# Optimization experiments

Measured on AMD Instinct MI355X. Metric: run time of the kernel, lower is better.

Reference implementation:

```python
import jax, jax.numpy as jnp
import numpy as np

N_WAY = 5
K_SHOT = 5
TEMPERATURE = 1.0
NEG = -1e9  # emulates 'column does not exist' for pad columns beyond umask_length
EPS = 1e-12  # matches torch F.normalize eps


def _l2n(x, axis):
    n = jnp.sqrt(jnp.sum(x * x, axis=axis, keepdims=True))
    return x / jnp.maximum(n, EPS)


def setup_inputs() -> dict:
    key = jax.random.key(0)
    k1, k2, k3, k4, k5 = jax.random.split(key, 5)
    b, c, h, w = 4, 64, 5, 5
    q, u = 75, 100
    support_xf = jax.random.normal(k1, (b, N_WAY * K_SHOT, c, h, w), jnp.float32)
    query_xf = jax.random.normal(k2, (b, q, c, h, w), jnp.float32)
    unlabeled_xf = jax.random.normal(k3, (b, u, c, h, w), jnp.float32)
    support_y = jax.random.randint(k4, (b, N_WAY * K_SHOT), 0, N_WAY)
    query_y = jax.random.randint(k5, (b, q), 0, N_WAY)
    return {"support_xf": support_xf, "support_y": support_y, "query_xf": query_xf,
            "query_y": query_y, "unlabeled_xf": unlabeled_xf}


def _forward(support_xf, query_xf, unlabeled_xf, query_y):
    b, q, c, h, w = query_xf.shape
    M_s = K_SHOT * h * w
    unl = unlabeled_xf.reshape(b, -1, c, h, w)
    u = unl.shape[1]
    M_u = u * h * w
    # pooled unlabeled local descriptors, flattened in (u, h, w) order -> [b, c, M_u]
    unl_feat = unl.transpose(0, 2, 1, 3, 4).reshape(b, c, M_u)
    # support -> [b, n_way, c, k_shot*h*w]
    sup = support_xf.reshape(b, N_WAY, K_SHOT, c, h, w).transpose(0, 1, 3, 2, 4, 5).reshape(b, N_WAY, c, M_s)
    # cosine similarity unlabeled -> support: [b, n_way, M_u, M_s]
    u2s = jnp.einsum('bwcn,bcm->bwmn', _l2n(sup, 2), _l2n(unl_feat, 1))
    pool = u2s.transpose(0, 2, 1, 3).reshape(b, M_u, N_WAY * M_s)
    s_nearest = jnp.argmax(pool, axis=1)          # per support loc: nearest unlabeled loc
    u_nearest = jnp.argmax(pool, axis=2)          # per unlabeled loc: nearest support loc
    mutual = jnp.take_along_axis(s_nearest, u_nearest, axis=1) == jnp.arange(M_u)[None, :]  # [b, M_u]
    # class with max similarity per unlabeled location
    cls = jnp.argmax(jnp.max(u2s, axis=-1), axis=1)  # [b, M_u]
    umask = jax.nn.one_hot(cls, N_WAY, dtype=jnp.float32).transpose(0, 2, 1) \
            * mutual[:, None, :].astype(jnp.float32)  # [b, n_way, M_u]
    counts = umask.sum(-1)                          # [b, n_way]
    L = counts.max()                                # umask_length (traced)
    # stream compaction via stable argsort of the 0/1 mask (preserves original order)
    order = jnp.argsort(-umask, axis=-1)            # jnp.argsort is stable
    pts = unl_feat.transpose(0, 2, 1)               # [b, M_u, c]
    gath = jnp.take_along_axis(pts[:, None, :, :], order[..., None], axis=2)  # [b, n_way, M_u, c]
    valid = (jnp.arange(M_u)[None, None, :] < counts[:, :, None]).astype(jnp.float32)
    comp = gath * valid[..., None]                  # rows beyond count are zeros (as in torch)
    s_cat = jnp.concatenate([sup, comp.transpose(0, 1, 3, 2)], axis=-1)  # [b, n_way, c, M_s+M_u]
    M_tot = M_s + M_u
    qn = _l2n(query_xf.reshape(b, q, c, h * w), 2)
    scn = _l2n(s_cat, 2)
    sim = jnp.einsum('bqcm,bwcn->bqwmn', qn, scn)   # [b, q, n_way, M_q, M_tot]
    sim = (sim + 1.0) * 0.5                          # FourLayer_64F branch
    # columns beyond umask_length don't exist in the torch dense tensor -> exclude from maxes
    pad = jnp.arange(M_tot)[None, None, None, None, :] >= (M_s + L)
    sim = jnp.where(pad, NEG, sim)
    M_q = h * w
    qm = sim.transpose(0, 1, 3, 2, 4).reshape(b, q, M_q, N_WAY * M_tot)
    support_nearest = jnp.argmax(qm, axis=2)        # [b, q, n_way*M_tot]
    query_nearest = jnp.argmax(qm, axis=3)          # [b, q, M_q]
    g = jnp.take_along_axis(support_nearest, query_nearest, axis=2)
    q_mask = (g == jnp.arange(M_q)[None, None, :]).astype(sim.dtype)  # mutual NN mask
    query_value = (jnp.max(sim, axis=-1) * q_mask[:, :, None, :]).sum(-1)  # [b, q, n_way]
    logits = query_value.reshape(b * q, N_WAY) / TEMPERATURE
    y = query_y.reshape(b * q)
    logp = jax.nn.log_softmax(logits, axis=-1)
    loss = -jnp.take_along_axis(logp, y[:, None], axis=1).mean()
    return loss


def reference(support_xf, support_y, query_xf, query_y, unlabeled_xf):
    return _forward(support_xf, query_xf, unlabeled_xf, query_y)
```

## Files before the change

kernel.cpp:

```cpp
#include <hip/hip_runtime.h>

#define NEGINF (-1e30f)

constexpr size_t OF_UNL  = 0;
constexpr size_t OF_SUP  = OF_UNL  + (size_t)4*2500*64;
constexpr size_t OF_SUPT = OF_SUP  + (size_t)4*5*125*64;
constexpr size_t OF_QT   = OF_SUPT + (size_t)4*5*64*128;
constexpr size_t OF_ROWV = OF_QT   + (size_t)300*28*64;
constexpr size_t OF_ROWI = OF_ROWV + (size_t)4*5*8*2500;
constexpr size_t OF_CVI  = OF_ROWI + (size_t)4*5*8*2500;
constexpr size_t OF_CMP  = OF_CVI  + (size_t)4*5*125*20*2;
constexpr size_t OF_CNT  = OF_CMP  + (size_t)4*5*2500;
constexpr size_t OF_UNEAR= OF_CNT  + 20;
constexpr size_t OF_SNEAR= OF_UNEAR+ 10000;
constexpr size_t OF_BV   = OF_SNEAR+ 2500;
constexpr size_t OF_BP   = OF_BV   + 37500;
constexpr size_t OF_AMX  = OF_BP   + 37500;

typedef __attribute__((ext_vector_type(4)))  float f4s;
typedef __attribute__((ext_vector_type(16))) float f16s;

__global__ __launch_bounds__(256) void knorm(
    const float* __restrict__ sup, const float* __restrict__ qry,
    const float* __restrict__ unl,
    float* __restrict__ unl_n, float* __restrict__ sup_n,
    float* __restrict__ supT, float* __restrict__ qt)
{
    int tid = threadIdx.x;
    int lane = tid & 63, wv = tid >> 6;
    int unit = blockIdx.x * 4 + wv;

    __shared__ float ls[4][1600];
    __shared__ float scl[4][32];

    const float* src;
    float* dstT;
    float* dst2 = nullptr;
    int dst2_shot = 0;
    bool isq = false;

    if (unit < 400) {
        int b = unit / 100, u = unit % 100;
        src  = unl + (size_t)unit * 1600;
        dstT = unl_n + ((size_t)(b * 2500 + u * 25)) * 64;
    } else if (unit < 500) {
        int idx2 = unit - 400;
        int b = idx2 / 25, r = idx2 % 25;
        int w = r / 5, shot = r % 5;
        src  = sup + (size_t)(b * 25 + r) * 1600;
        dstT = sup_n + ((size_t)(b * 625 + w * 125 + shot * 25)) * 64;
        dst2 = supT + ((size_t)(b * 5 + w) * 64) * 128;
        dst2_shot = shot * 25;
    } else {
        int bq = unit - 500;
        src  = qry + (size_t)bq * 1600;
        dstT = qt + (size_t)bq * 1792;
        isq = true;
    }

    const float4* s4 = (const float4*)src;
#pragma unroll
    for (int k = 0; k < 7; ++k) {
        int idx = k * 64 + lane;
        if (idx < 400) *(float4*)&ls[wv][idx * 4] = s4[idx];
    }
    __syncthreads();

    if (lane < 25) {
        int hw = lane;
        float p[16];
#pragma unroll
        for (int sub = 0; sub < 16; ++sub) {
            float s = 0.f;
#pragma unroll
            for (int j = 0; j < 4; ++j) {
                float v = ls[wv][(sub * 4 + j) * 25 + hw];
                s += v * v;
            }
            p[sub] = s;
        }
#pragma unroll
        for (int st = 1; st < 16; st <<= 1)
#pragma unroll
            for (int i = 0; i < 16; i += 2 * st)
                p[i] = p[i] + p[i + st];
        scl[wv][hw] = 1.f / fmaxf(sqrtf(p[0]), 1e-12f);
    }
    __syncthreads();

    float4* d4 = (float4*)dstT;
#pragma unroll
    for (int k = 0; k < 7; ++k) {
        int idx = k * 64 + lane;
        if (idx < 400) {
            int f = idx * 4;
            int r_ = f >> 6;
            int c0 = f & 63;
            float m = scl[wv][r_];
            float4 o;
            o.x = ls[wv][ c0      * 25 + r_] * m;
            o.y = ls[wv][(c0 + 1) * 25 + r_] * m;
            o.z = ls[wv][(c0 + 2) * 25 + r_] * m;
            o.w = ls[wv][(c0 + 3) * 25 + r_] * m;
            d4[idx] = o;
        }
    }
    if (isq) {
        if (lane < 48) d4[400 + lane] = make_float4(0.f, 0.f, 0.f, 0.f);
    }
    if (dst2) {
#pragma unroll
        for (int k = 0; k < 25; ++k) {
            int idx = k * 64 + lane;
            int c = idx / 25, hw2 = idx % 25;
            dst2[(size_t)c * 128 + dst2_shot + hw2] = ls[wv][idx] * scl[wv][hw2];
        }
    }
}

#define KB2(C) { \
    f16s s0, s1; \
    asm volatile("s_load_dwordx16 %0, %[b], %c[o0]\n\t" \
                 "s_load_dwordx16 %1, %[b], %c[o1]\n\t" \
                 "s_waitcnt lgkmcnt(0)" \
                 : "=s"(s0), "=s"(s1) \
                 : [b]"s"(sbp), [o0]"i"((C)*512), [o1]"i"((C)*512+512)); \
    float2 uv = *(const float2*)&uls[ml * 66 + (C)]; \
    acc[0]  = fmaf(uv.x, s0[0],  fmaf(uv.y, s1[0],  acc[0])); \
    acc[1]  = fmaf(uv.x, s0[1],  fmaf(uv.y, s1[1],  acc[1])); \
    acc[2]  = fmaf(uv.x, s0[2],  fmaf(uv.y, s1[2],  acc[2])); \
    acc[3]  = fmaf(uv.x, s0[3],  fmaf(uv.y, s1[3],  acc[3])); \
    acc[4]  = fmaf(uv.x, s0[4],  fmaf(uv.y, s1[4],  acc[4])); \
    acc[5]  = fmaf(uv.x, s0[5],  fmaf(uv.y, s1[5],  acc[5])); \
    acc[6]  = fmaf(uv.x, s0[6],  fmaf(uv.y, s1[6],  acc[6])); \
    acc[7]  = fmaf(uv.x, s0[7],  fmaf(uv.y, s1[7],  acc[7])); \
    acc[8]  = fmaf(uv.x, s0[8],  fmaf(uv.y, s1[8],  acc[8])); \
    acc[9]  = fmaf(uv.x, s0[9],  fmaf(uv.y, s1[9],  acc[9])); \
    acc[10] = fmaf(uv.x, s0[10], fmaf(uv.y, s1[10], acc[10])); \
    acc[11] = fmaf(uv.x, s0[11], fmaf(uv.y, s1[11], acc[11])); \
    acc[12] = fmaf(uv.x, s0[12], fmaf(uv.y, s1[12], acc[12])); \
    acc[13] = fmaf(uv.x, s0[13], fmaf(uv.y, s1[13], acc[13])); \
    acc[14] = fmaf(uv.x, s0[14], fmaf(uv.y, s1[14], acc[14])); \
    acc[15] = fmaf(uv.x, s0[15], fmaf(uv.y, s1[15], acc[15])); }
#define KB8(C) KB2(C) KB2((C)+2) KB2((C)+4) KB2((C)+6)

__global__ __launch_bounds__(256) void kb(
    const float* __restrict__ unl_n, const float* __restrict__ supT,
    float* __restrict__ rowv, int* __restrict__ rowi, float* __restrict__ colvi)
{
    int bid = blockIdx.x;
    int nc = bid & 3;
    int mb = (bid >> 2) % 20;
    int bw = bid / 80;
    int b  = bw / 5;
    int tid = threadIdx.x;
    int lane = tid & 63, wv = tid >> 6;

    __shared__ float uls[128 * 66];
    __shared__ float sv_[4][32];
    __shared__ int   si_[4][32];

    int m0 = mb * 128;
    int n0 = nc * 32;

    for (int i = tid; i < 128 * 16; i += 256) {
        int row = i >> 4, c4 = (i & 15) * 4;
        int m = m0 + row;
        float4 x = make_float4(0.f, 0.f, 0.f, 0.f);
        if (m < 2500) x = *(const float4*)(unl_n + ((size_t)(b * 2500 + m)) * 64 + c4);
        *(float2*)&uls[row * 66 + c4]     = make_float2(x.x, x.y);
        *(float2*)&uls[row * 66 + c4 + 2] = make_float2(x.z, x.w);
    }
    __syncthreads();

    int ml = tid & 127;
    int m  = m0 + ml;
    int nh = tid >> 7;
    int nbase = nh * 16;
    int nbu = __builtin_amdgcn_readfirstlane(nbase);
    int nn_total = (125 - n0) < 32 ? (125 - n0) : 32;
    const float* sbp = supT + ((size_t)bw * 64) * 128 + n0 + nbu;

    float acc[16];
#pragma unroll
    for (int j = 0; j < 16; ++j) acc[j] = 0.f;

    KB8(0)  KB8(8)  KB8(16) KB8(24)
    KB8(32) KB8(40) KB8(48) KB8(56)

    int nnloc = nn_total - nbase;
    nnloc = nnloc < 0 ? 0 : (nnloc > 16 ? 16 : nnloc);
    float rbv = NEGINF; int rbi = 0;
    for (int j = 0; j < nnloc; ++j)
        if (acc[j] > rbv) { rbv = acc[j]; rbi = n0 + nbase + j; }
    if (m < 2500) {
        int ck = nc * 2 + nh;
        rowv[((size_t)bw * 8 + ck) * 2500 + m] = rbv;
        rowi[((size_t)bw * 8 + ck) * 2500 + m] = rbi;
    }

#pragma unroll
    for (int j = 0; j < 16; ++j) {
        float v = (m < 2500 && (nbase + j) < nn_total) ? acc[j] : NEGINF;
        float vm = v;
#pragma unroll
        for (int s2 = 1; s2 < 64; s2 <<= 1) vm = fmaxf(vm, __shfl_xor(vm, s2));
        unsigned long long msk = __ballot(v == vm);
        int first = __ffsll((unsigned long long)msk) - 1;
        if (lane == 0) { sv_[wv][nbase + j] = vm; si_[wv][nbase + j] = m0 + (wv & 1) * 64 + first; }
    }
    __syncthreads();
    if (tid < nn_total) {
        int w0 = (tid < 16) ? 0 : 2;
        float v = sv_[w0][tid];     int vi = si_[w0][tid];
        float v2 = sv_[w0 + 1][tid]; int i2 = si_[w0 + 1][tid];
        if (v2 > v || (v2 == v && i2 < vi)) { v = v2; vi = i2; }
        float* cv = colvi + ((((size_t)bw) * 125 + (n0 + tid)) * 20 + mb) * 2;
        cv[0] = v; ((int*)cv)[1] = vi;
    }
}

__global__ __launch_bounds__(64) void kmerge(
    const float* __restrict__ rowv, const int* __restrict__ rowi,
    const float* __restrict__ colvi,
    int* __restrict__ unear, int* __restrict__ snear)
{
    int it = blockIdx.x * 64 + threadIdx.x;
    if (it < 10000) {
        int b = it / 2500, m = it % 2500;
        float bv = NEGINF; int bi = 0;
#pragma unroll
        for (int w = 0; w < 5; ++w) {
#pragma unroll
            for (int ck = 0; ck < 8; ++ck) {
                size_t o = (((size_t)(b * 5 + w)) * 8 + ck) * 2500 + m;
                float v = rowv[o];
                if (v > bv) { bv = v; bi = w * 125 + rowi[o]; }
            }
        }
        unear[it] = bi;
    } else if (it < 12500) {
        int idx = it - 10000;
        const float* p = colvi + (size_t)idx * 40;
        float bv = NEGINF; int bi = 0x7fffffff;
        for (int mb2 = 0; mb2 < 20; ++mb2) {
            float v = p[mb2 * 2]; int vi = ((const int*)p)[mb2 * 2 + 1];
            if (v > bv || (v == bv && vi < bi)) { bv = v; bi = vi; }
        }
        snear[idx] = bi;
    }
}

__global__ __launch_bounds__(256) void kcmp(
    const int* __restrict__ unear, const int* __restrict__ snear,
    int* __restrict__ cmp, int* __restrict__ cntg)
{
    int p = blockIdx.x;
    int b = p / 5, way = p % 5;
    int tid = threadIdx.x, lane = tid & 63, wv = tid >> 6;
    __shared__ unsigned long long masks[40];
    __shared__ int base[40];

    for (int ch = wv; ch < 40; ch += 4) {
        int m = ch * 64 + lane;
        bool ok = false;
        if (m < 2500) {
            int un = unear[b * 2500 + m];
            ok = (un / 125 == way) && (snear[b * 625 + un] == m);
        }
        unsigned long long msk = __ballot(ok ? 1 : 0);
        if (lane == 0) masks[ch] = msk;
    }
    __syncthreads();
    if (tid == 0) {
        int s = 0;
        for (int ch = 0; ch < 40; ++ch) { base[ch] = s; s += __popcll(masks[ch]); }
        cntg[p] = s;
    }
    __syncthreads();
    for (int ch = wv; ch < 40; ch += 4) {
        unsigned long long msk = masks[ch];
        if ((msk >> lane) & 1ull) {
            int pre = __popcll(msk & ((1ull << lane) - 1ull));
            cmp[(size_t)p * 2500 + base[ch] + pre] = ch * 64 + lane;
        }
    }
}

#define QLOAD(CG, Q0,Q1,Q2,Q3,Q4,Q5,Q6) \
  asm volatile( \
    "s_load_dwordx4 %0, %[b], %c[o0]\n\t" \
    "s_load_dwordx4 %1, %[b], %c[o1]\n\t" \
    "s_load_dwordx4 %2, %[b], %c[o2]\n\t" \
    "s_load_dwordx4 %3, %[b], %c[o3]\n\t" \
    "s_load_dwordx4 %4, %[b], %c[o4]\n\t" \
    "s_load_dwordx4 %5, %[b], %c[o5]\n\t" \
    "s_load_dwordx4 %6, %[b], %c[o6]\n\t" \
    "s_waitcnt lgkmcnt(0)" \
    : "=s"(Q0), "=s"(Q1), "=s"(Q2), "=s"(Q3), "=s"(Q4), "=s"(Q5), "=s"(Q6) \
    : [b]"s"(qbp), \
      [o0]"i"((CG)*16 + 0*256), [o1]"i"((CG)*16 + 1*256), \
      [o2]"i"((CG)*16 + 2*256), [o3]"i"((CG)*16 + 3*256), \
      [o4]"i"((CG)*16 + 4*256), [o5]"i"((CG)*16 + 5*256), \
      [o6]"i"((CG)*16 + 6*256))

#define CGSTEP(CG) { \
    f4s q0,q1,q2,q3,q4,q5,q6; \
    QLOAD(CG, q0,q1,q2,q3,q4,q5,q6); \
    float4 cl = *(const float4*)&cls[lane * 68 + (CG) * 4]; \
    acc[0]=fmaf(q0.x,cl.x,fmaf(q0.y,cl.y,fmaf(q0.z,cl.z,fmaf(q0.w,cl.w,acc[0])))); \
    acc[1]=fmaf(q1.x,cl.x,fmaf(q1.y,cl.y,fmaf(q1.z,cl.z,fmaf(q1.w,cl.w,acc[1])))); \
    acc[2]=fmaf(q2.x,cl.x,fmaf(q2.y,cl.y,fmaf(q2.z,cl.z,fmaf(q2.w,cl.w,acc[2])))); \
    acc[3]=fmaf(q3.x,cl.x,fmaf(q3.y,cl.y,fmaf(q3.z,cl.z,fmaf(q3.w,cl.w,acc[3])))); \
    acc[4]=fmaf(q4.x,cl.x,fmaf(q4.y,cl.y,fmaf(q4.z,cl.z,fmaf(q4.w,cl.w,acc[4])))); \
    acc[5]=fmaf(q5.x,cl.x,fmaf(q5.y,cl.y,fmaf(q5.z,cl.z,fmaf(q5.w,cl.w,acc[5])))); \
    acc[6]=fmaf(q6.x,cl.x,fmaf(q6.y,cl.y,fmaf(q6.z,cl.z,fmaf(q6.w,cl.w,acc[6])))); }

__global__ __launch_bounds__(256) void kc1(
    const float* __restrict__ qt, const float* __restrict__ sup_n,
    const float* __restrict__ unl_n, const int* __restrict__ cmp,
    const int* __restrict__ cntg,
    float* __restrict__ bvg, int* __restrict__ bpg,
    unsigned char* __restrict__ amaxg)
{
    int bid = blockIdx.x;
    int w = bid % 5, bq = bid / 5;
    int b = bq / 75;
    int tid = threadIdx.x;
    int lane = tid & 63;
    int wvu = __builtin_amdgcn_readfirstlane(tid >> 6);
    int pbw = b * 5 + w;

    int L = 0;
#pragma unroll
    for (int i = 0; i < 20; ++i) { int v = cntg[i]; L = L > v ? L : v; }
    int cntw = 0, wb = 0;
#pragma unroll
    for (int w2 = 0; w2 < 5; ++w2) {
        int c2 = cntg[b * 5 + w2];
        if (w2 < w) wb += 125 + c2;
        if (w2 == w) cntw = c2;
    }
    int cw = 125 + cntw;

    __shared__ float cls[64 * 68];
    __shared__ float amxv[4][64];
    __shared__ int   amxg_[4][64];
    __shared__ float redv[25];
    __shared__ int   redn[25];

    const float* qbp = qt + ((size_t)bq * 28 + wvu * 7) * 64;

    float rv[7]; int rn[7];
#pragma unroll
    for (int j = 0; j < 7; ++j) { rv[j] = NEGINF; rn[j] = 0x7fffffff; }

    int nb = (cw + 63) >> 6;

    for (int b4 = 0; b4 < nb; ++b4) {
        if (b4 > 0 && tid < 64) {
            int n = (b4 - 1) * 64 + tid;
            if (n < cw) {
                float v = amxv[0][tid]; int g = amxg_[0][tid];
#pragma unroll
                for (int g2 = 1; g2 < 4; ++g2)
                    if (amxv[g2][tid] > v) { v = amxv[g2][tid]; g = amxg_[g2][tid]; }
                amaxg[(size_t)bq * 3200 + (wb + n)] = (unsigned char)g;
            }
        }
#pragma unroll
        for (int k = 0; k < 4; ++k) {
            int i = tid + k * 256;
            int row = i >> 4, ch = i & 15;
            int n = b4 * 64 + row;
            float4 x = make_float4(0.f, 0.f, 0.f, 0.f);
            if (n < cw) {
                const float* cp;
                if (n < 125) cp = sup_n + (((size_t)pbw) * 125 + n) * 64;
                else { int m = cmp[((size_t)pbw) * 2500 + (n - 125)];
                       cp = unl_n + ((size_t)(b * 2500 + m)) * 64; }
                x = *(const float4*)(cp + ch * 4);
            }
            *(float4*)&cls[row * 68 + ch * 4] = x;
        }
        __syncthreads();

        float acc[7];
#pragma unroll
        for (int j = 0; j < 7; ++j) acc[j] = 0.f;

        CGSTEP(0);  CGSTEP(1);  CGSTEP(2);  CGSTEP(3);
        CGSTEP(4);  CGSTEP(5);  CGSTEP(6);  CGSTEP(7);
        CGSTEP(8);  CGSTEP(9);  CGSTEP(10); CGSTEP(11);
        CGSTEP(12); CGSTEP(13); CGSTEP(14); CGSTEP(15);

        bool colvalid = (b4 * 64 + lane) < cw;
        float cmax = NEGINF; int cam = 0;
#pragma unroll
        for (int j = 0; j < 7; ++j) {
            int mq = wvu * 7 + j;
            float s = (acc[j] + 1.0f) * 0.5f;
            float sm = (colvalid && mq < 25) ? s : NEGINF;
            if (sm > cmax) { cmax = sm; cam = mq; }
            float vm = sm;
#pragma unroll
            for (int t = 1; t < 64; t <<= 1) vm = fmaxf(vm, __shfl_xor(vm, t));
            unsigned long long msk = __ballot(sm == vm);
            int first = __ffsll(msk) - 1;
            if (vm > rv[j]) { rv[j] = vm; rn[j] = b4 * 64 + first; }
        }
        amxv[wvu][lane] = cmax; amxg_[wvu][lane] = cam;
        __syncthreads();
    }

    if (tid < 64) {
        int n = (nb - 1) * 64 + tid;
        if (n < cw) {
            float v = amxv[0][tid]; int g = amxg_[0][tid];
#pragma unroll
            for (int g2 = 1; g2 < 4; ++g2)
                if (amxv[g2][tid] > v) { v = amxv[g2][tid]; g = amxg_[g2][tid]; }
            amaxg[(size_t)bq * 3200 + (wb + n)] = (unsigned char)g;
        }
    }
    if (lane == 0) {
#pragma unroll
        for (int j = 0; j < 7; ++j) {
            int mq = wvu * 7 + j;
            if (mq < 25) { redv[mq] = rv[j]; redn[mq] = rn[j]; }
        }
    }
    __syncthreads();

    if (tid < 25) {
        float v = redv[tid]; int nn = redn[tid];
        int p = ((w * 2625 + nn) << 12) | (wb + nn);
        if (L > cntw) {
            int pp = ((w * 2625 + 125 + cntw) << 12) | 0xFFF;
            if (0.5f > v || (0.5f == v && pp < p)) { v = 0.5f; p = pp; }
        }
        size_t o = ((size_t)bq * 5 + w) * 25 + tid;
        bvg[o] = v; bpg[o] = p;
    }
}

__global__ __launch_bounds__(64) void kce(
    const float* __restrict__ bvg, const int* __restrict__ bpg,
    const unsigned char* __restrict__ amaxg, const int* __restrict__ qy,
    float* __restrict__ out)
{
    int bq = blockIdx.x;
    int tid = threadIdx.x;
    __shared__ float qmask[25];
    __shared__ float lg[5];
    if (tid < 25) {
        float v = NEGINF; int p = 0x7fffffff;
#pragma unroll
        for (int w = 0; w < 5; ++w) {
            size_t o = ((size_t)bq * 5 + w) * 25 + tid;
            float v2 = bvg[o]; int p2 = bpg[o];
            if (v2 > v || (v2 == v && p2 < p)) { v = v2; p = p2; }
        }
        int pos = p & 0xFFF;
        int g = (pos == 0xFFF) ? 0 : (int)amaxg[(size_t)bq * 3200 + pos];
        qmask[tid] = (g == tid) ? 1.0f : 0.0f;
    }
    __syncthreads();
    if (tid < 5) {
        float s = 0.f;
#pragma unroll
        for (int mq = 0; mq < 25; ++mq)
            s += bvg[((size_t)bq * 5 + tid) * 25 + mq] * qmask[mq];
        lg[tid] = s;
    }
    __syncthreads();
    if (tid == 0) {
        int y = qy[bq];
        float mx = lg[0];
#pragma unroll
        for (int w = 1; w < 5; ++w) mx = fmaxf(mx, lg[w]);
        float se = 0.f;
#pragma unroll
        for (int w = 0; w < 5; ++w) se += expf(lg[w] - mx);
        float loss = -(lg[y] - mx - logf(se));
        atomicAdd(out, loss * (1.0f / 300.0f));
    }
}

extern "C" void kernel_launch(void* const* d_in, const int* in_sizes, int n_in,
                              void* d_out, int out_size, void* d_ws, size_t ws_size,
                              hipStream_t stream)
{
    const float* sup = (const float*)d_in[0];
    const float* qry = (const float*)d_in[2];
    const int*   qy  = (const int*)d_in[3];
    const float* unl = (const float*)d_in[4];

    float* ws    = (float*)d_ws;
    float* unl_n = ws + OF_UNL;
    float* sup_n = ws + OF_SUP;
    float* supT  = ws + OF_SUPT;
    float* qt    = ws + OF_QT;
    float* rowv  = ws + OF_ROWV;
    int*   rowi  = (int*)(ws + OF_ROWI);
    float* colvi = ws + OF_CVI;
    int*   cmp   = (int*)(ws + OF_CMP);
    int*   cntg  = (int*)(ws + OF_CNT);
    int*   unear = (int*)(ws + OF_UNEAR);
    int*   snear = (int*)(ws + OF_SNEAR);
    float* bvg   = ws + OF_BV;
    int*   bpg   = (int*)(ws + OF_BP);
    unsigned char* amaxg = (unsigned char*)(ws + OF_AMX);

    hipMemsetAsync(d_out, 0, sizeof(float), stream);

    hipLaunchKernelGGL(knorm, dim3(200), dim3(256), 0, stream,
                       sup, qry, unl, unl_n, sup_n, supT, qt);
    hipLaunchKernelGGL(kb, dim3(1600), dim3(256), 0, stream,
                       unl_n, supT, rowv, rowi, colvi);
    hipLaunchKernelGGL(kmerge, dim3(196), dim3(64), 0, stream,
                       rowv, rowi, colvi, unear, snear);
    hipLaunchKernelGGL(kcmp, dim3(20), dim3(256), 0, stream,
                       unear, snear, cmp, cntg);
    hipLaunchKernelGGL(kc1, dim3(1500), dim3(256), 0, stream,
                       qt, sup_n, unl_n, cmp, cntg, bvg, bpg, amaxg);
    hipLaunchKernelGGL(kce, dim3(300), dim3(64), 0, stream,
                       bvg, bpg, amaxg, qy, (float*)d_out);
}
```

Before: 180.4 us.

## Fuse six kernel launches into one persistent cooperative kernel with grid syncs

Merges the normalize, support-unlabeled similarity, merge, compaction, query-similarity and cross-entropy kernels into a single persistent kernel. Each stage runs as a grid-stride loop separated by grid-wide syncs, and the output memset moves into the kernel. The goal is to remove per-launch overhead and the gaps between the small kernels. In exchange, the grid is capped at 1024 blocks with 256 threads each, so the 1600- and 1500-block stages must loop, and every grid sync adds a device-wide barrier cost.

```diff
diff --git a/kernel.cpp b/kernel.cpp
--- a/kernel.cpp
+++ b/kernel.cpp
@@ -1,4 +1,7 @@
 #include <hip/hip_runtime.h>
+#include <hip/hip_cooperative_groups.h>
+
+namespace cg = cooperative_groups;
 
 #define NEGINF (-1e30f)
 
@@ -19,104 +22,6 @@
 
 typedef __attribute__((ext_vector_type(4)))  float f4s;
 typedef __attribute__((ext_vector_type(16))) float f16s;
-
-__global__ __launch_bounds__(256) void knorm(
-    const float* __restrict__ sup, const float* __restrict__ qry,
-    const float* __restrict__ unl,
-    float* __restrict__ unl_n, float* __restrict__ sup_n,
-    float* __restrict__ supT, float* __restrict__ qt)
-{
-    int tid = threadIdx.x;
-    int lane = tid & 63, wv = tid >> 6;
-    int unit = blockIdx.x * 4 + wv;
-
-    __shared__ float ls[4][1600];
-    __shared__ float scl[4][32];
-
-    const float* src;
-    float* dstT;
-    float* dst2 = nullptr;
-    int dst2_shot = 0;
-    bool isq = false;
-
-    if (unit < 400) {
-        int b = unit / 100, u = unit % 100;
-        src  = unl + (size_t)unit * 1600;
-        dstT = unl_n + ((size_t)(b * 2500 + u * 25)) * 64;
-    } else if (unit < 500) {
-        int idx2 = unit - 400;
-        int b = idx2 / 25, r = idx2 % 25;
-        int w = r / 5, shot = r % 5;
-        src  = sup + (size_t)(b * 25 + r) * 1600;
-        dstT = sup_n + ((size_t)(b * 625 + w * 125 + shot * 25)) * 64;
-        dst2 = supT + ((size_t)(b * 5 + w) * 64) * 128;
-        dst2_shot = shot * 25;
-    } else {
-        int bq = unit - 500;
-        src  = qry + (size_t)bq * 1600;
-        dstT = qt + (size_t)bq * 1792;
-        isq = true;
-    }
-
-    const float4* s4 = (const float4*)src;
-#pragma unroll
-    for (int k = 0; k < 7; ++k) {
-        int idx = k * 64 + lane;
-        if (idx < 400) *(float4*)&ls[wv][idx * 4] = s4[idx];
-    }
-    __syncthreads();
-
-    if (lane < 25) {
-        int hw = lane;
-        float p[16];
-#pragma unroll
-        for (int sub = 0; sub < 16; ++sub) {
-            float s = 0.f;
-#pragma unroll
-            for (int j = 0; j < 4; ++j) {
-                float v = ls[wv][(sub * 4 + j) * 25 + hw];
-                s += v * v;
-            }
-            p[sub] = s;
-        }
-#pragma unroll
-        for (int st = 1; st < 16; st <<= 1)
-#pragma unroll
-            for (int i = 0; i < 16; i += 2 * st)
-                p[i] = p[i] + p[i + st];
-        scl[wv][hw] = 1.f / fmaxf(sqrtf(p[0]), 1e-12f);
-    }
-    __syncthreads();
-
-    float4* d4 = (float4*)dstT;
-#pragma unroll
-    for (int k = 0; k < 7; ++k) {
-        int idx = k * 64 + lane;
-        if (idx < 400) {
-            int f = idx * 4;
-            int r_ = f >> 6;
-            int c0 = f & 63;
-            float m = scl[wv][r_];
-            float4 o;
-            o.x = ls[wv][ c0      * 25 + r_] * m;
-            o.y = ls[wv][(c0 + 1) * 25 + r_] * m;
-            o.z = ls[wv][(c0 + 2) * 25 + r_] * m;
-            o.w = ls[wv][(c0 + 3) * 25 + r_] * m;
-            d4[idx] = o;
-        }
-    }
-    if (isq) {
-        if (lane < 48) d4[400 + lane] = make_float4(0.f, 0.f, 0.f, 0.f);
-    }
-    if (dst2) {
-#pragma unroll
-        for (int k = 0; k < 25; ++k) {
-            int idx = k * 64 + lane;
-            int c = idx / 25, hw2 = idx % 25;
-            dst2[(size_t)c * 128 + dst2_shot + hw2] = ls[wv][idx] * scl[wv][hw2];
-        }
-    }
-}
 
 #define KB2(C) { \
     f16s s0, s1; \
@@ -144,149 +49,6 @@
     acc[15] = fmaf(uv.x, s0[15], fmaf(uv.y, s1[15], acc[15])); }
 #define KB8(C) KB2(C) KB2((C)+2) KB2((C)+4) KB2((C)+6)
 
-__global__ __launch_bounds__(256) void kb(
-    const float* __restrict__ unl_n, const float* __restrict__ supT,
-    float* __restrict__ rowv, int* __restrict__ rowi, float* __restrict__ colvi)
-{
-    int bid = blockIdx.x;
-    int nc = bid & 3;
-    int mb = (bid >> 2) % 20;
-    int bw = bid / 80;
-    int b  = bw / 5;
-    int tid = threadIdx.x;
-    int lane = tid & 63, wv = tid >> 6;
-
-    __shared__ float uls[128 * 66];
-    __shared__ float sv_[4][32];
-    __shared__ int   si_[4][32];
-
-    int m0 = mb * 128;
-    int n0 = nc * 32;
-
-    for (int i = tid; i < 128 * 16; i += 256) {
-        int row = i >> 4, c4 = (i & 15) * 4;
-        int m = m0 + row;
-        float4 x = make_float4(0.f, 0.f, 0.f, 0.f);
-        if (m < 2500) x = *(const float4*)(unl_n + ((size_t)(b * 2500 + m)) * 64 + c4);
-        *(float2*)&uls[row * 66 + c4]     = make_float2(x.x, x.y);
-        *(float2*)&uls[row * 66 + c4 + 2] = make_float2(x.z, x.w);
-    }
-    __syncthreads();
-
-    int ml = tid & 127;
-    int m  = m0 + ml;
-    int nh = tid >> 7;
-    int nbase = nh * 16;
-    int nbu = __builtin_amdgcn_readfirstlane(nbase);
-    int nn_total = (125 - n0) < 32 ? (125 - n0) : 32;
-    const float* sbp = supT + ((size_t)bw * 64) * 128 + n0 + nbu;
-
-    float acc[16];
-#pragma unroll
-    for (int j = 0; j < 16; ++j) acc[j] = 0.f;
-
-    KB8(0)  KB8(8)  KB8(16) KB8(24)
-    KB8(32) KB8(40) KB8(48) KB8(56)
-
-    int nnloc = nn_total - nbase;
-    nnloc = nnloc < 0 ? 0 : (nnloc > 16 ? 16 : nnloc);
-    float rbv = NEGINF; int rbi = 0;
-    for (int j = 0; j < nnloc; ++j)
-        if (acc[j] > rbv) { rbv = acc[j]; rbi = n0 + nbase + j; }
-    if (m < 2500) {
-        int ck = nc * 2 + nh;
-        rowv[((size_t)bw * 8 + ck) * 2500 + m] = rbv;
-        rowi[((size_t)bw * 8 + ck) * 2500 + m] = rbi;
-    }
-
-#pragma unroll
-    for (int j = 0; j < 16; ++j) {
-        float v = (m < 2500 && (nbase + j) < nn_total) ? acc[j] : NEGINF;
-        float vm = v;
-#pragma unroll
-        for (int s2 = 1; s2 < 64; s2 <<= 1) vm = fmaxf(vm, __shfl_xor(vm, s2));
-        unsigned long long msk = __ballot(v == vm);
-        int first = __ffsll((unsigned long long)msk) - 1;
-        if (lane == 0) { sv_[wv][nbase + j] = vm; si_[wv][nbase + j] = m0 + (wv & 1) * 64 + first; }
-    }
-    __syncthreads();
-    if (tid < nn_total) {
-        int w0 = (tid < 16) ? 0 : 2;
-        float v = sv_[w0][tid];     int vi = si_[w0][tid];
-        float v2 = sv_[w0 + 1][tid]; int i2 = si_[w0 + 1][tid];
-        if (v2 > v || (v2 == v && i2 < vi)) { v = v2; vi = i2; }
-        float* cv = colvi + ((((size_t)bw) * 125 + (n0 + tid)) * 20 + mb) * 2;
-        cv[0] = v; ((int*)cv)[1] = vi;
-    }
-}
-
-__global__ __launch_bounds__(64) void kmerge(
-    const float* __restrict__ rowv, const int* __restrict__ rowi,
-    const float* __restrict__ colvi,
-    int* __restrict__ unear, int* __restrict__ snear)
-{
-    int it = blockIdx.x * 64 + threadIdx.x;
-    if (it < 10000) {
-        int b = it / 2500, m = it % 2500;
-        float bv = NEGINF; int bi = 0;
-#pragma unroll
-        for (int w = 0; w < 5; ++w) {
-#pragma unroll
-            for (int ck = 0; ck < 8; ++ck) {
-                size_t o = (((size_t)(b * 5 + w)) * 8 + ck) * 2500 + m;
-                float v = rowv[o];
-                if (v > bv) { bv = v; bi = w * 125 + rowi[o]; }
-            }
-        }
-        unear[it] = bi;
-    } else if (it < 12500) {
-        int idx = it - 10000;
-        const float* p = colvi + (size_t)idx * 40;
-        float bv = NEGINF; int bi = 0x7fffffff;
-        for (int mb2 = 0; mb2 < 20; ++mb2) {
-            float v = p[mb2 * 2]; int vi = ((const int*)p)[mb2 * 2 + 1];
-            if (v > bv || (v == bv && vi < bi)) { bv = v; bi = vi; }
-        }
-        snear[idx] = bi;
-    }
-}
-
-__global__ __launch_bounds__(256) void kcmp(
-    const int* __restrict__ unear, const int* __restrict__ snear,
-    int* __restrict__ cmp, int* __restrict__ cntg)
-{
-    int p = blockIdx.x;
-    int b = p / 5, way = p % 5;
-    int tid = threadIdx.x, lane = tid & 63, wv = tid >> 6;
-    __shared__ unsigned long long masks[40];
-    __shared__ int base[40];
-
-    for (int ch = wv; ch < 40; ch += 4) {
-        int m = ch * 64 + lane;
-        bool ok = false;
-        if (m < 2500) {
-            int un = unear[b * 2500 + m];
-            ok = (un / 125 == way) && (snear[b * 625 + un] == m);
-        }
-        unsigned long long msk = __ballot(ok ? 1 : 0);
-        if (lane == 0) masks[ch] = msk;
-    }
-    __syncthreads();
-    if (tid == 0) {
-        int s = 0;
-        for (int ch = 0; ch < 40; ++ch) { base[ch] = s; s += __popcll(masks[ch]); }
-        cntg[p] = s;
-    }
-    __syncthreads();
-    for (int ch = wv; ch < 40; ch += 4) {
-        unsigned long long msk = masks[ch];
-        if ((msk >> lane) & 1ull) {
-            int pre = __popcll(msk & ((1ull << lane) - 1ull));
-            cmp[(size_t)p * 2500 + base[ch] + pre] = ch * 64 + lane;
-        }
-    }
-}
-
 #define QLOAD(CG, Q0,Q1,Q2,Q3,Q4,Q5,Q6) \
   asm volatile( \
     "s_load_dwordx4 %0, %[b], %c[o0]\n\t" \
@@ -316,187 +78,14 @@
     acc[5]=fmaf(q5.x,cl.x,fmaf(q5.y,cl.y,fmaf(q5.z,cl.z,fmaf(q5.w,cl.w,acc[5])))); \
     acc[6]=fmaf(q6.x,cl.x,fmaf(q6.y,cl.y,fmaf(q6.z,cl.z,fmaf(q6.w,cl.w,acc[6])))); }
 
-__global__ __launch_bounds__(256) void kc1(
-    const float* __restrict__ qt, const float* __restrict__ sup_n,
-    const float* __restrict__ unl_n, const int* __restrict__ cmp,
-    const int* __restrict__ cntg,
-    float* __restrict__ bvg, int* __restrict__ bpg,
-    unsigned char* __restrict__ amaxg)
+__global__ __launch_bounds__(256, 4) void fused(
+    const float* __restrict__ sup, const float* __restrict__ qry,
+    const float* __restrict__ unl, const int* __restrict__ qy,
+    float* __restrict__ out, float* __restrict__ ws)
 {
-    int bid = blockIdx.x;
-    int w = bid % 5, bq = bid / 5;
-    int b = bq / 75;
-    int tid = threadIdx.x;
-    int lane = tid & 63;
-    int wvu = __builtin_amdgcn_readfirstlane(tid >> 6);
-    int pbw = b * 5 + w;
-
-    int L = 0;
-#pragma unroll
-    for (int i = 0; i < 20; ++i) { int v = cntg[i]; L = L > v ? L : v; }
-    int cntw = 0, wb = 0;
-#pragma unroll
-    for (int w2 = 0; w2 < 5; ++w2) {
-        int c2 = cntg[b * 5 + w2];
-        if (w2 < w) wb += 125 + c2;
-        if (w2 == w) cntw = c2;
-    }
-    int cw = 125 + cntw;
-
-    __shared__ float cls[64 * 68];
-    __shared__ float amxv[4][64];
-    __shared__ int   amxg_[4][64];
-    __shared__ float redv[25];
-    __shared__ int   redn[25];
-
-    const float* qbp = qt + ((size_t)bq * 28 + wvu * 7) * 64;
-
-    float rv[7]; int rn[7];
-#pragma unroll
-    for (int j = 0; j < 7; ++j) { rv[j] = NEGINF; rn[j] = 0x7fffffff; }
-
-    int nb = (cw + 63) >> 6;
-
-    for (int b4 = 0; b4 < nb; ++b4) {
-        if (b4 > 0 && tid < 64) {
-            int n = (b4 - 1) * 64 + tid;
-            if (n < cw) {
-                float v = amxv[0][tid]; int g = amxg_[0][tid];
-#pragma unroll
-                for (int g2 = 1; g2 < 4; ++g2)
-                    if (amxv[g2][tid] > v) { v = amxv[g2][tid]; g = amxg_[g2][tid]; }
-                amaxg[(size_t)bq * 3200 + (wb + n)] = (unsigned char)g;
-            }
-        }
-#pragma unroll
-        for (int k = 0; k < 4; ++k) {
-            int i = tid + k * 256;
-            int row = i >> 4, ch = i & 15;
-            int n = b4 * 64 + row;
-            float4 x = make_float4(0.f, 0.f, 0.f, 0.f);
-            if (n < cw) {
-                const float* cp;
-                if (n < 125) cp = sup_n + (((size_t)pbw) * 125 + n) * 64;
-                else { int m = cmp[((size_t)pbw) * 2500 + (n - 125)];
-                       cp = unl_n + ((size_t)(b * 2500 + m)) * 64; }
-                x = *(const float4*)(cp + ch * 4);
-            }
-            *(float4*)&cls[row * 68 + ch * 4] = x;
-        }
-        __syncthreads();
-
-        float acc[7];
-#pragma unroll
-        for (int j = 0; j < 7; ++j) acc[j] = 0.f;
-
-        CGSTEP(0);  CGSTEP(1);  CGSTEP(2);  CGSTEP(3);
-        CGSTEP(4);  CGSTEP(5);  CGSTEP(6);  CGSTEP(7);
-        CGSTEP(8);  CGSTEP(9);  CGSTEP(10); CGSTEP(11);
-        CGSTEP(12); CGSTEP(13); CGSTEP(14); CGSTEP(15);
-
-        bool colvalid = (b4 * 64 + lane) < cw;
-        float cmax = NEGINF; int cam = 0;
-#pragma unroll
-        for (int j = 0; j < 7; ++j) {
-            int mq = wvu * 7 + j;
-            float s = (acc[j] + 1.0f) * 0.5f;
-            float sm = (colvalid && mq < 25) ? s : NEGINF;
-            if (sm > cmax) { cmax = sm; cam = mq; }
-            float vm = sm;
-#pragma unroll
-            for (int t = 1; t < 64; t <<= 1) vm = fmaxf(vm, __shfl_xor(vm, t));
-            unsigned long long msk = __ballot(sm == vm);
-            int first = __ffsll(msk) - 1;
-            if (vm > rv[j]) { rv[j] = vm; rn[j] = b4 * 64 + first; }
-        }
-        amxv[wvu][lane] = cmax; amxg_[wvu][lane] = cam;
-        __syncthreads();
-    }
-
-    if (tid < 64) {
-        int n = (nb - 1) * 64 + tid;
-        if (n < cw) {
-            float v = amxv[0][tid]; int g = amxg_[0][tid];
-#pragma unroll
-            for (int g2 = 1; g2 < 4; ++g2)
-                if (amxv[g2][tid] > v) { v = amxv[g2][tid]; g = amxg_[g2][tid]; }
-            amaxg[(size_t)bq * 3200 + (wb + n)] = (unsigned char)g;
-        }
-    }
-    if (lane == 0) {
-#pragma unroll
-        for (int j = 0; j < 7; ++j) {
-            int mq = wvu * 7 + j;
-            if (mq < 25) { redv[mq] = rv[j]; redn[mq] = rn[j]; }
-        }
-    }
-    __syncthreads();
-
-    if (tid < 25) {
-        float v = redv[tid]; int nn = redn[tid];
-        int p = ((w * 2625 + nn) << 12) | (wb + nn);
-        if (L > cntw) {
-            int pp = ((w * 2625 + 125 + cntw) << 12) | 0xFFF;
-            if (0.5f > v || (0.5f == v && pp < p)) { v = 0.5f; p = pp; }
-        }
-        size_t o = ((size_t)bq * 5 + w) * 25 + tid;
-        bvg[o] = v; bpg[o] = p;
-    }
-}
-
-__global__ __launch_bounds__(64) void kce(
-    const float* __restrict__ bvg, const int* __restrict__ bpg,
-    const unsigned char* __restrict__ amaxg, const int* __restrict__ qy,
-    float* __restrict__ out)
-{
-    int bq = blockIdx.x;
-    int tid = threadIdx.x;
-    __shared__ float qmask[25];
-    __shared__ float lg[5];
-    if (tid < 25) {
-        float v = NEGINF; int p = 0x7fffffff;
-#pragma unroll
-        for (int w = 0; w < 5; ++w) {
-            size_t o = ((size_t)bq * 5 + w) * 25 + tid;
-            float v2 = bvg[o]; int p2 = bpg[o];
-            if (v2 > v || (v2 == v && p2 < p)) { v = v2; p = p2; }
-        }
-        int pos = p & 0xFFF;
-        int g = (pos == 0xFFF) ? 0 : (int)amaxg[(size_t)bq * 3200 + pos];
-        qmask[tid] = (g == tid) ? 1.0f : 0.0f;
-    }
-    __syncthreads();
-    if (tid < 5) {
-        float s = 0.f;
-#pragma unroll
-        for (int mq = 0; mq < 25; ++mq)
-            s += bvg[((size_t)bq * 5 + tid) * 25 + mq] * qmask[mq];
-        lg[tid] = s;
-    }
-    __syncthreads();
-    if (tid == 0) {
-        int y = qy[bq];
-        float mx = lg[0];
-#pragma unroll
-        for (int w = 1; w < 5; ++w) mx = fmaxf(mx, lg[w]);
-        float se = 0.f;
-#pragma unroll
-        for (int w = 0; w < 5; ++w) se += expf(lg[w] - mx);
-        float loss = -(lg[y] - mx - logf(se));
-        atomicAdd(out, loss * (1.0f / 300.0f));
-    }
-}
-
-extern "C" void kernel_launch(void* const* d_in, const int* in_sizes, int n_in,
-                              void* d_out, int out_size, void* d_ws, size_t ws_size,
-                              hipStream_t stream)
-{
-    const float* sup = (const float*)d_in[0];
-    const float* qry = (const float*)d_in[2];
-    const int*   qy  = (const int*)d_in[3];
-    const float* unl = (const float*)d_in[4];
-
-    float* ws    = (float*)d_ws;
+    __shared__ __align__(16) float smem[8704];
+    cg::grid_group gridg = cg::this_grid();
+
     float* unl_n = ws + OF_UNL;
     float* sup_n = ws + OF_SUP;
     float* supT  = ws + OF_SUPT;
@@ -512,18 +101,406 @@
     int*   bpg   = (int*)(ws + OF_BP);
     unsigned char* amaxg = (unsigned char*)(ws + OF_AMX);
 
-    hipMemsetAsync(d_out, 0, sizeof(float), stream);
-
-    hipLaunchKernelGGL(knorm, dim3(200), dim3(256), 0, stream,
-                       sup, qry, unl, unl_n, sup_n, supT, qt);
-    hipLaunchKernelGGL(kb, dim3(1600), dim3(256), 0, stream,
-                       unl_n, supT, rowv, rowi, colvi);
-    hipLaunchKernelGGL(kmerge, dim3(196), dim3(64), 0, stream,
-                       rowv, rowi, colvi, unear, snear);
-    hipLaunchKernelGGL(kcmp, dim3(20), dim3(256), 0, stream,
-                       unear, snear, cmp, cntg);
-    hipLaunchKernelGGL(kc1, dim3(1500), dim3(256), 0, stream,
-                       qt, sup_n, unl_n, cmp, cntg, bvg, bpg, amaxg);
-    hipLaunchKernelGGL(kce, dim3(300), dim3(64), 0, stream,
-                       bvg, bpg, amaxg, qy, (float*)d_out);
+    int tid = threadIdx.x;
+    int lane = tid & 63, wv = tid >> 6;
+    int bid = blockIdx.x, nblk = gridDim.x;
+
+    if (bid == 0 && tid == 0) *out = 0.f;
+    for (int u0 = bid; u0 < 200; u0 += nblk) {
+        int unit = u0 * 4 + wv;
+        float* lsw  = smem + wv * 1600;
+        float* sclw = smem + 6400 + wv * 32;
+
+        const float* src;
+        float* dstT; float* dst2 = nullptr; int dst2_shot = 0; bool isq = false;
+        if (unit < 400) {
+            int b = unit / 100, u = unit % 100;
+            src  = unl + (size_t)unit * 1600;
+            dstT = unl_n + ((size_t)(b * 2500 + u * 25)) * 64;
+        } else if (unit < 500) {
+            int idx2 = unit - 400;
+            int b = idx2 / 25, r = idx2 % 25;
+            int w = r / 5, shot = r % 5;
+            src  = sup + (size_t)(b * 25 + r) * 1600;
+            dstT = sup_n + ((size_t)(b * 625 + w * 125 + shot * 25)) * 64;
+            dst2 = supT + ((size_t)(b * 5 + w) * 64) * 128;
+            dst2_shot = shot * 25;
+        } else {
+            int bq = unit - 500;
+            src  = qry + (size_t)bq * 1600;
+            dstT = qt + (size_t)bq * 1792;
+            isq = true;
+        }
+
+        const float4* s4 = (const float4*)src;
+#pragma unroll
+        for (int k = 0; k < 7; ++k) {
+            int idx = k * 64 + lane;
+            if (idx < 400) *(float4*)&lsw[idx * 4] = s4[idx];
+        }
+        __syncthreads();
+        if (lane < 25) {
+            int hw = lane;
+            float p[16];
+#pragma unroll
+            for (int sub = 0; sub < 16; ++sub) {
+                float s = 0.f;
+#pragma unroll
+                for (int j = 0; j < 4; ++j) {
+                    float v = lsw[(sub * 4 + j) * 25 + hw];
+                    s += v * v;
+                }
+                p[sub] = s;
+            }
+#pragma unroll
+            for (int st = 1; st < 16; st <<= 1)
+#pragma unroll
+                for (int i = 0; i < 16; i += 2 * st)
+                    p[i] = p[i] + p[i + st];
+            sclw[hw] = 1.f / fmaxf(sqrtf(p[0]), 1e-12f);
+        }
+        __syncthreads();
+        float4* d4 = (float4*)dstT;
+#pragma unroll
+        for (int k = 0; k < 7; ++k) {
+            int idx = k * 64 + lane;
+            if (idx < 400) {
+                int f = idx * 4;
+                int r_ = f >> 6;
+                int c0 = f & 63;
+                float m = sclw[r_];
+                float4 o;
+                o.x = lsw[ c0      * 25 + r_] * m;
+                o.y = lsw[(c0 + 1) * 25 + r_] * m;
+                o.z = lsw[(c0 + 2) * 25 + r_] * m;
+                o.w = lsw[(c0 + 3) * 25 + r_] * m;
+                d4[idx] = o;
+            }
+        }
+        if (isq && lane < 48) d4[400 + lane] = make_float4(0.f, 0.f, 0.f, 0.f);
+        if (dst2) {
+#pragma unroll
+            for (int k = 0; k < 25; ++k) {
+                int idx = k * 64 + lane;
+                int c = idx / 25, hw2 = idx % 25;
+                dst2[(size_t)c * 128 + dst2_shot + hw2] = lsw[idx] * sclw[hw2];
+            }
+        }
+        __syncthreads();
+    }
+    gridg.sync();
+
+    for (int vb = bid; vb < 1600; vb += nblk) {
+        int nc = vb & 3;
+        int mb = (vb >> 2) % 20;
+        int bw = vb / 80;
+        int b  = bw / 5;
+        float* uls = smem;
+        float* sv_f = smem + 8448;
+        int*   si_  = (int*)(smem + 8448 + 128);
+
+        int m0 = mb * 128;
+        int n0 = nc * 32;
+
+        for (int i = tid; i < 128 * 16; i += 256) {
+            int row = i >> 4, c4 = (i & 15) * 4;
+            int m = m0 + row;
+            float4 x = make_float4(0.f, 0.f, 0.f, 0.f);
+            if (m < 2500) x = *(const float4*)(unl_n + ((size_t)(b * 2500 + m)) * 64 + c4);
+            *(float2*)&uls[row * 66 + c4]     = make_float2(x.x, x.y);
+            *(float2*)&uls[row * 66 + c4 + 2] = make_float2(x.z, x.w);
+        }
+        __syncthreads();
+
+        int ml = tid & 127;
+        int m  = m0 + ml;
+        int nh = tid >> 7;
+        int nbase = nh * 16;
+        int nbu = __builtin_amdgcn_readfirstlane(nbase);
+        int nn_total = (125 - n0) < 32 ? (125 - n0) : 32;
+        const float* sbp = supT + ((size_t)bw * 64) * 128 + n0 + nbu;
+
+        float acc[16];
+#pragma unroll
+        for (int j = 0; j < 16; ++j) acc[j] = 0.f;
+
+        KB8(0)  KB8(8)  KB8(16) KB8(24)
+        KB8(32) KB8(40) KB8(48) KB8(56)
+
+        int nnloc = nn_total - nbase;
+        nnloc = nnloc < 0 ? 0 : (nnloc > 16 ? 16 : nnloc);
+        float rbv = NEGINF; int rbi = 0;
+        for (int j = 0; j < nnloc; ++j)
+            if (acc[j] > rbv) { rbv = acc[j]; rbi = n0 + nbase + j; }
+        if (m < 2500) {
+            int ck = nc * 2 + nh;
+            rowv[((size_t)bw * 8 + ck) * 2500 + m] = rbv;
+            rowi[((size_t)bw * 8 + ck) * 2500 + m] = rbi;
+        }
+
+#pragma unroll
+        for (int j = 0; j < 16; ++j) {
+            float v = (m < 2500 && (nbase + j) < nn_total) ? acc[j] : NEGINF;
+            float vm = v;
+#pragma unroll
+            for (int s2 = 1; s2 < 64; s2 <<= 1) vm = fmaxf(vm, __shfl_xor(vm, s2));
+            unsigned long long msk = __ballot(v == vm);
+            int first = __ffsll((unsigned long long)msk) - 1;
+            if (lane == 0) { sv_f[wv * 32 + nbase + j] = vm; si_[wv * 32 + nbase + j] = m0 + (wv & 1) * 64 + first; }
+        }
+        __syncthreads();
+        if (tid < nn_total) {
+            int w0 = (tid < 16) ? 0 : 2;
+            float v = sv_f[w0 * 32 + tid];       int vi = si_[w0 * 32 + tid];
+            float v2 = sv_f[(w0 + 1) * 32 + tid]; int i2 = si_[(w0 + 1) * 32 + tid];
+            if (v2 > v || (v2 == v && i2 < vi)) { v = v2; vi = i2; }
+            float* cv = colvi + ((((size_t)bw) * 125 + (n0 + tid)) * 20 + mb) * 2;
+            cv[0] = v; ((int*)cv)[1] = vi;
+        }
+        __syncthreads();
+    }
+    gridg.sync();
+
+    for (int it = bid * 256 + tid; it < 12500; it += nblk * 256) {
+        if (it < 10000) {
+            int b = it / 2500, m = it % 2500;
+            float bv = NEGINF; int bi = 0;
+#pragma unroll
+            for (int w = 0; w < 5; ++w) {
+#pragma unroll
+                for (int ck = 0; ck < 8; ++ck) {
+                    size_t o = (((size_t)(b * 5 + w)) * 8 + ck) * 2500 + m;
+                    float v = rowv[o];
+                    if (v > bv) { bv = v; bi = w * 125 + rowi[o]; }
+                }
+            }
+            unear[it] = bi;
+        } else {
+            int idx = it - 10000;
+            const float* p = colvi + (size_t)idx * 40;
+            float bv = NEGINF; int bi = 0x7fffffff;
+            for (int mb2 = 0; mb2 < 20; ++mb2) {
+                float v = p[mb2 * 2]; int vi = ((const int*)p)[mb2 * 2 + 1];
+                if (v > bv || (v == bv && vi < bi)) { bv = v; bi = vi; }
+            }
+            snear[idx] = bi;
+        }
+    }
+    gridg.sync();
+
+    for (int p = bid; p < 20; p += nblk) {
+        int b = p / 5, way = p % 5;
+        unsigned long long* masks = (unsigned long long*)smem;
+        int* base = (int*)(smem + 80);
+
+        for (int ch = wv; ch < 40; ch += 4) {
+            int m = ch * 64 + lane;
+            bool ok = false;
+            if (m < 2500) {
+                int un = unear[b * 2500 + m];
+                ok = (un / 125 == way) && (snear[b * 625 + un] == m);
+            }
+            unsigned long long msk = __ballot(ok ? 1 : 0);
+            if (lane == 0) masks[ch] = msk;
+        }
+        __syncthreads();
+        if (tid == 0) {
+            int s = 0;
+            for (int ch = 0; ch < 40; ++ch) { base[ch] = s; s += __popcll(masks[ch]); }
+            cntg[p] = s;
+        }
+        __syncthreads();
+        for (int ch = wv; ch < 40; ch += 4) {
+            unsigned long long msk = masks[ch];
+            if ((msk >> lane) & 1ull) {
+                int pre = __popcll(msk & ((1ull << lane) - 1ull));
+                cmp[(size_t)p * 2500 + base[ch] + pre] = ch * 64 + lane;
+            }
+        }
+        __syncthreads();
+    }
+    gridg.sync();
+
+    for (int vb = bid; vb < 1500; vb += nblk) {
+        int w = vb % 5, bq = vb / 5;
+        int b = bq / 75;
+        int wvu = __builtin_amdgcn_readfirstlane(tid >> 6);
+        int pbw = b * 5 + w;
+
+        int L = 0;
+#pragma unroll
+        for (int i = 0; i < 20; ++i) { int v = cntg[i]; L = L > v ? L : v; }
+        int cntw = 0, wb = 0;
+#pragma unroll
+        for (int w2 = 0; w2 < 5; ++w2) {
+            int c2 = cntg[b * 5 + w2];
+            if (w2 < w) wb += 125 + c2;
+            if (w2 == w) cntw = c2;
+        }
+        int cw = 125 + cntw;
+
+        float* cls   = smem;
+        float* amxv  = smem + 4352;
+        int*   amxg_ = (int*)(smem + 4608);
+        float* redv  = smem + 4864;
+        int*   redn  = (int*)(smem + 4889);
+
+        const float* qbp = qt + ((size_t)bq * 28 + wvu * 7) * 64;
+
+        float rv[7]; int rn[7];
+#pragma unroll
+        for (int j = 0; j < 7; ++j) { rv[j] = NEGINF; rn[j] = 0x7fffffff; }
+
+        int nb = (cw + 63) >> 6;
+
+        for (int b4 = 0; b4 < nb; ++b4) {
+            if (b4 > 0 && tid < 64) {
+                int n = (b4 - 1) * 64 + tid;
+                if (n < cw) {
+                    float v = amxv[tid]; int g = amxg_[tid];
+#pragma unroll
+                    for (int g2 = 1; g2 < 4; ++g2)
+                        if (amxv[g2 * 64 + tid] > v) { v = amxv[g2 * 64 + tid]; g = amxg_[g2 * 64 + tid]; }
+                    amaxg[(size_t)bq * 3200 + (wb + n)] = (unsigned char)g;
+                }
+            }
+#pragma unroll
+            for (int k = 0; k < 4; ++k) {
+                int i = tid + k * 256;
+                int row = i >> 4, ch = i & 15;
+                int n = b4 * 64 + row;
+                float4 x = make_float4(0.f, 0.f, 0.f, 0.f);
+                if (n < cw) {
+                    const float* cp;
+                    if (n < 125) cp = sup_n + (((size_t)pbw) * 125 + n) * 64;
+                    else { int m = cmp[((size_t)pbw) * 2500 + (n - 125)];
+                           cp = unl_n + ((size_t)(b * 2500 + m)) * 64; }
+                    x = *(const float4*)(cp + ch * 4);
+                }
+                *(float4*)&cls[row * 68 + ch * 4] = x;
+            }
+            __syncthreads();
+
+            float acc[7];
+#pragma unroll
+            for (int j = 0; j < 7; ++j) acc[j] = 0.f;
+
+            CGSTEP(0);  CGSTEP(1);  CGSTEP(2);  CGSTEP(3);
+            CGSTEP(4);  CGSTEP(5);  CGSTEP(6);  CGSTEP(7);
+            CGSTEP(8);  CGSTEP(9);  CGSTEP(10); CGSTEP(11);
+            CGSTEP(12); CGSTEP(13); CGSTEP(14); CGSTEP(15);
+
+            bool colvalid = (b4 * 64 + lane) < cw;
+            float cmax = NEGINF; int cam = 0;
+#pragma unroll
+            for (int j = 0; j < 7; ++j) {
+                int mq = wvu * 7 + j;
+                float s = (acc[j] + 1.0f) * 0.5f;
+                float sm = (colvalid && mq < 25) ? s : NEGINF;
+                if (sm > cmax) { cmax = sm; cam = mq; }
+                float vm = sm;
+#pragma unroll
+                for (int t = 1; t < 64; t <<= 1) vm = fmaxf(vm, __shfl_xor(vm, t));
+                unsigned long long msk = __ballot(sm == vm);
+                int first = __ffsll(msk) - 1;
+                if (vm > rv[j]) { rv[j] = vm; rn[j] = b4 * 64 + first; }
+            }
+            amxv[wvu * 64 + lane] = cmax; amxg_[wvu * 64 + lane] = cam;
+            __syncthreads();
+        }
+
+        if (tid < 64) {
+            int n = (nb - 1) * 64 + tid;
+            if (n < cw) {
+                float v = amxv[tid]; int g = amxg_[tid];
+#pragma unroll
+                for (int g2 = 1; g2 < 4; ++g2)
+                    if (amxv[g2 * 64 + tid] > v) { v = amxv[g2 * 64 + tid]; g = amxg_[g2 * 64 + tid]; }
+                amaxg[(size_t)bq * 3200 + (wb + n)] = (unsigned char)g;
+            }
+        }
+        if (lane == 0) {
+#pragma unroll
+            for (int j = 0; j < 7; ++j) {
+                int mq = wvu * 7 + j;
+                if (mq < 25) { redv[mq] = rv[j]; redn[mq] = rn[j]; }
+            }
+        }
+        __syncthreads();
+
+        if (tid < 25) {
+            float v = redv[tid]; int nn = redn[tid];
+            int p = ((w * 2625 + nn) << 12) | (wb + nn);
+            if (L > cntw) {
+                int pp = ((w * 2625 + 125 + cntw) << 12) | 0xFFF;
+                if (0.5f > v || (0.5f == v && pp < p)) { v = 0.5f; p = pp; }
+            }
+            size_t o = ((size_t)bq * 5 + w) * 25 + tid;
+            bvg[o] = v; bpg[o] = p;
+        }
+        __syncthreads();
+    }
+    gridg.sync();
+
+    for (int bq = bid; bq < 300; bq += nblk) {
+        float* qmask = smem;
+        float* lg    = smem + 25;
+        if (tid < 25) {
+            float v = NEGINF; int p = 0x7fffffff;
+#pragma unroll
+            for (int w = 0; w < 5; ++w) {
+                size_t o = ((size_t)bq * 5 + w) * 25 + tid;
+                float v2 = bvg[o]; int p2 = bpg[o];
+                if (v2 > v || (v2 == v && p2 < p)) { v = v2; p = p2; }
+            }
+            int pos = p & 0xFFF;
+            int g = (pos == 0xFFF) ? 0 : (int)amaxg[(size_t)bq * 3200 + pos];
+            qmask[tid] = (g == tid) ? 1.0f : 0.0f;
+        }
+        __syncthreads();
+        if (tid < 5) {
+            float s = 0.f;
+#pragma unroll
+            for (int mq = 0; mq < 25; ++mq)
+                s += bvg[((size_t)bq * 5 + tid) * 25 + mq] * qmask[mq];
+            lg[tid] = s;
+        }
+        __syncthreads();
+        if (tid == 0) {
+            int y = qy[bq];
+            float mx = lg[0];
+#pragma unroll
+            for (int w = 1; w < 5; ++w) mx = fmaxf(mx, lg[w]);
+            float se = 0.f;
+#pragma unroll
+            for (int w = 0; w < 5; ++w) se += expf(lg[w] - mx);
+            float loss = -(lg[y] - mx - logf(se));
+            atomicAdd(out, loss * (1.0f / 300.0f));
+        }
+        __syncthreads();
+    }
 }
+
+extern "C" void kernel_launch(void* const* d_in, const int* in_sizes, int n_in,
+                              void* d_out, int out_size, void* d_ws, size_t ws_size,
+                              hipStream_t stream)
+{
+    const float* sup = (const float*)d_in[0];
+    const float* qry = (const float*)d_in[2];
+    const int*   qy  = (const int*)d_in[3];
+    const float* unl = (const float*)d_in[4];
+    float* outp = (float*)d_out;
+    float* ws   = (float*)d_ws;
+
+    static int maxb = 0;
+    if (maxb == 0) {
+        hipOccupancyMaxActiveBlocksPerMultiprocessor(&maxb, fused, 256, 0);
+        if (maxb < 1) maxb = 1;
+    }
+    int grid = maxb * 256;
+    if (grid > 1024) grid = 1024;
+
+    void* args[] = { (void*)&sup, (void*)&qry, (void*)&unl,
+                     (void*)&qy, (void*)&outp, (void*)&ws };
+    hipLaunchCooperativeKernel(fused, dim3(grid), dim3(256), args, 0, stream);
+}
```

Result: slower. 507.1 us (+181.0%).
